# Optimization experiments

Hardware: AMD Instinct MI355X
Metric: run time of the kernel (lower is better)

Reference implementation:

```python
import jax, jax.numpy as jnp
import numpy as np
import math

EMBED_DIM = 1024
NUM_HEADS = 16
HEAD_DIM = EMBED_DIM // NUM_HEADS
BATCH = 2
SEQ = 2048


def setup_inputs() -> dict:
    key = jax.random.key(0)
    ks = jax.random.split(key, 9)
    s = 1.0 / math.sqrt(EMBED_DIM)
    return {
        "x": jax.random.normal(ks[0], (BATCH, SEQ, EMBED_DIM), jnp.float32),
        "Wq": jax.random.normal(ks[1], (EMBED_DIM, EMBED_DIM), jnp.float32) * s,
        "bq": jnp.zeros((EMBED_DIM,), jnp.float32),
        "Wk": jax.random.normal(ks[2], (EMBED_DIM, EMBED_DIM), jnp.float32) * s,
        "bk": jnp.zeros((EMBED_DIM,), jnp.float32),
        "Wv": jax.random.normal(ks[3], (EMBED_DIM, EMBED_DIM), jnp.float32) * s,
        "bv": jnp.zeros((EMBED_DIM,), jnp.float32),
        "Wo": jax.random.normal(ks[4], (EMBED_DIM, EMBED_DIM), jnp.float32) * s,
        "bo": jnp.zeros((EMBED_DIM,), jnp.float32),
    }


def _rope_tables(seq_len, dim, dtype):
    inv_freq = 1.0 / (10000.0 ** (jnp.arange(0, dim, 2, dtype=jnp.float32) / dim))
    t = jnp.arange(seq_len, dtype=jnp.float32)
    freqs = jnp.einsum("i,j->ij", t, inv_freq)          # [S, D/2]
    emb = jnp.concatenate([freqs, freqs], axis=-1)       # [S, D]
    return jnp.cos(emb).astype(dtype), jnp.sin(emb).astype(dtype)


def _rotate_half(x):
    x1, x2 = jnp.split(x, 2, axis=-1)
    return jnp.concatenate([-x2, x1], axis=-1)


def _apply_rope(x, cos, sin):
    # x: [B, S, H, D]; cos/sin: [S, D] -> broadcast over batch & heads
    cos = cos[None, :, None, :]
    sin = sin[None, :, None, :]
    return x * cos + _rotate_half(x) * sin


def reference(x, Wq, bq, Wk, bk, Wv, bv, Wo, bo):
    B, S, E = x.shape
    H, D = NUM_HEADS, HEAD_DIM
    q = (x @ Wq + bq).reshape(B, S, H, D)
    k = (x @ Wk + bk).reshape(B, S, H, D)
    v = (x @ Wv + bv).reshape(B, S, H, D)
    cos, sin = _rope_tables(S, D, x.dtype)
    q = _apply_rope(q, cos, sin)
    k = _apply_rope(k, cos, sin)
    scale = 1.0 / math.sqrt(D)
    # scores: [B, H, S, S]
    scores = jnp.einsum("bqhd,bkhd->bhqk", q, k) * scale
    attn = jax.nn.softmax(scores, axis=-1)
    ctx = jnp.einsum("bhqk,bkhd->bqhd", attn, v).reshape(B, S, E)
    return ctx @ Wo + bo
```

## Files before the change

kernel.cpp:

```cpp
#include <hip/hip_runtime.h>
#include <math.h>

#define B_ 2
#define S_ 2048
#define E_ 1024
#define H_ 16
#define D_ 64
#define M_ (B_*S_)

typedef _Float16 f16x8  __attribute__((ext_vector_type(8)));
typedef _Float16 f16x4v __attribute__((ext_vector_type(4)));
typedef __fp16   h16x2  __attribute__((ext_vector_type(2)));
typedef float    f32x4  __attribute__((ext_vector_type(4)));

__device__ __forceinline__ ushort f2h(float f) {
    _Float16 h = (_Float16)f;
    return __builtin_bit_cast(ushort, h);
}

__device__ __forceinline__ void gload_lds16(const ushort* g, ushort* l) {
    __builtin_amdgcn_global_load_lds(
        (const __attribute__((address_space(1))) unsigned int*)g,
        (__attribute__((address_space(3))) unsigned int*)l, 16, 0, 0);
}

__device__ __forceinline__ float exp2_fast(float x) {
    return __builtin_amdgcn_exp2f(x);
}

__global__ void prep_kernel(const float* __restrict__ x,
                            const float* __restrict__ W0, const float* __restrict__ W1,
                            const float* __restrict__ W2, const float* __restrict__ W3,
                            ushort* __restrict__ xf, ushort* __restrict__ WT,
                            float* __restrict__ ct, float* __restrict__ st)
{
    const int bid = blockIdx.x;
    const int tid = threadIdx.x;
    __shared__ float tile[32][33];

    if (bid < 4096) {
        const int z = bid >> 10, rem = bid & 1023;
        const int k0 = (rem >> 5) * 32, nb = (rem & 31) * 32;
        const float* W = (z == 0) ? W0 : (z == 1) ? W1 : (z == 2) ? W2 : W3;
        const size_t zoff = (size_t)z * E_ * E_;
        const int tx = tid & 31, ty = tid >> 5;
        #pragma unroll
        for (int i = 0; i < 4; i++) {
            int r = i * 8 + ty;
            tile[r][tx] = W[(size_t)(k0 + r) * E_ + nb + tx];
        }
        __syncthreads();
        #pragma unroll
        for (int i = 0; i < 4; i++) {
            int r = i * 8 + ty;
            WT[zoff + (size_t)(nb + r) * E_ + k0 + tx] = f2h(tile[tx][r]);
        }
    } else if (bid < 8192) {
        const int i = (bid - 4096) * 1024 + tid * 4;
        float4 v = *(const float4*)&x[i];
        *(ushort4*)&xf[i] = make_ushort4(f2h(v.x), f2h(v.y), f2h(v.z), f2h(v.w));
    } else {
        const int i = (bid - 8192) * 256 + tid;
        const int j = i & 31, pos = i >> 5;
        float invf = (float)pow(10000.0, -(double)j / 32.0);
        float ang  = (float)pos * invf;
        ct[i] = (float)cos((double)ang);
        st[i] = (float)sin((double)ang);
    }
}

#define GBM 128
#define GBN 128
#define GBK 32
#define LOG2E 1.44269504088896340736f

__global__ __launch_bounds__(256, 3)
void gemm_f16(const ushort* __restrict__ A, const ushort* __restrict__ WTp,
              const float* __restrict__ b0, const float* __restrict__ b1,
              const float* __restrict__ b2,
              const float* __restrict__ ct, const float* __restrict__ st,
              ushort* __restrict__ outQ, ushort* __restrict__ outK,
              ushort* __restrict__ outV, float* __restrict__ outF,
              int force_mode)
{
    __shared__ __align__(16) ushort lA[3][GBM * GBK];
    __shared__ __align__(16) ushort lB[3][GBN * GBK];

    const int tid  = threadIdx.x;
    const int wv   = tid >> 6, lane = tid & 63;
    const int c    = lane & 15, qd = lane >> 4;
    const int rh   = wv >> 1, chn = wv & 1;

    const int mode = (force_mode >= 0) ? force_mode : (int)blockIdx.z;
    const size_t zoff = (force_mode >= 0) ? 0 : (size_t)blockIdx.z * (E_ * E_);
    const ushort* Bt = WTp + zoff;

    const int m0 = (blockIdx.x & 31) * GBM;
    const int n0 = (blockIdx.x >> 5) * GBN;

    const ushort* gsrc = (wv < 2) ? A : Bt;
    const int rowbase = ((wv < 2) ? m0 : n0) + (wv & 1) * 64;
    const int lofs = (wv & 1) * 64 * GBK;
    const int srow = lane >> 2;
    const int soct = (lane & 3) * 8;

    f32x4 acc[4][4] = {};

    #pragma unroll
    for (int pt = 0; pt < 2; pt++) {
        ushort* dst = ((wv < 2) ? &lA[pt][0] : &lB[pt][0]) + lofs;
        const int k0i = pt * GBK;
        #pragma unroll
        for (int cc = 0; cc < 4; cc++) {
            const ushort* g = gsrc + (size_t)(rowbase + cc * 16 + srow) * E_ + k0i + soct;
            gload_lds16(g, dst + cc * 512);
        }
    }
    __builtin_amdgcn_s_waitcnt(0x0F74);
    __builtin_amdgcn_s_barrier();

    for (int t = 0; t < E_ / GBK; t++) {
        if (t + 2 < E_ / GBK) {
            const int bi = (t + 2) % 3;
            const int k0i = (t + 2) * GBK;
            ushort* dst = ((wv < 2) ? &lA[bi][0] : &lB[bi][0]) + lofs;
            #pragma unroll
            for (int cc = 0; cc < 4; cc++) {
                const ushort* g = gsrc + (size_t)(rowbase + cc * 16 + srow) * E_ + k0i + soct;
                gload_lds16(g, dst + cc * 512);
            }
        }

        const ushort* Ab = lA[t % 3];
        const ushort* Bb = lB[t % 3];

        f16x8 af[4], bf[4];
        #pragma unroll
        for (int mt = 0; mt < 4; mt++)
            af[mt] = *(const f16x8*)&Ab[(rh * 64 + mt * 16 + c) * GBK + qd * 8];
        #pragma unroll
        for (int nt = 0; nt < 4; nt++)
            bf[nt] = *(const f16x8*)&Bb[(chn * 64 + nt * 16 + c) * GBK + qd * 8];
        #pragma unroll
        for (int mt = 0; mt < 4; mt++)
            #pragma unroll
            for (int nt = 0; nt < 4; nt++)
                acc[mt][nt] = __builtin_amdgcn_mfma_f32_16x16x32_f16(af[mt], bf[nt], acc[mt][nt], 0, 0, 0);

        if (t < E_ / GBK - 2) {
            __builtin_amdgcn_s_waitcnt(0x0F74);
            __builtin_amdgcn_s_barrier();
        } else if (t == E_ / GBK - 2) {
            __builtin_amdgcn_s_waitcnt(0x0F70);
            __builtin_amdgcn_s_barrier();
        }
    }

    const float* bias = (mode == 0) ? b0 : (mode == 1) ? b1 : (mode == 2) ? b2 : b0;
    const int colbase = n0 + chn * 64;

    if (mode == 3) {
        #pragma unroll
        for (int mt = 0; mt < 4; mt++)
            #pragma unroll
            for (int r = 0; r < 4; r++) {
                const int row = m0 + rh * 64 + mt * 16 + qd * 4 + r;
                #pragma unroll
                for (int nt = 0; nt < 4; nt++) {
                    const int col = colbase + nt * 16 + c;
                    outF[(size_t)row * E_ + col] = acc[mt][nt][r] + bias[col];
                }
            }
    } else if (mode == 2) {
        const int hd = colbase >> 6;
        const int xr = (c >> 2) & 3;
        #pragma unroll
        for (int mt = 0; mt < 4; mt++)
            #pragma unroll
            for (int r = 0; r < 4; r++) {
                const int row = m0 + rh * 64 + mt * 16 + qd * 4 + r;
                const int bb = row >> 11, sl = row & (S_ - 1);
                const int g  = sl >> 5, k32 = sl & 31;
                const int q2 = (k32 >> 2) & 3, kh = k32 >> 4, kj = k32 & 3;
                const size_t base = (size_t)(bb * H_ + hd) * (S_ * D_)
                                  + g * 2048 + ((q2 ^ xr) << 3) + kh * 4 + kj;
                #pragma unroll
                for (int nt = 0; nt < 4; nt++) {
                    const int d = nt * 16 + c;
                    outV[base + (size_t)d * 32] = f2h(acc[mt][nt][r] + bias[colbase + d]);
                }
            }
    } else {
        ushort* O = (mode == 0) ? outQ : outK;
        const float sc = (mode == 0) ? 0.125f * LOG2E : 1.0f;
        #pragma unroll
        for (int mt = 0; mt < 4; mt++)
            #pragma unroll
            for (int r = 0; r < 4; r++) {
                const int row = m0 + rh * 64 + mt * 16 + qd * 4 + r;
                const int pos = row & (S_ - 1);
                const int sw = row & 7;
                #pragma unroll
                for (int p = 0; p < 2; p++) {
                    const int j32 = p * 16 + c;
                    const float cth = ct[pos * 32 + j32], sth = st[pos * 32 + j32];
                    const float v1 = acc[mt][p][r]     + bias[colbase + p * 16 + c];
                    const float v2 = acc[mt][p + 2][r] + bias[colbase + (p + 2) * 16 + c];
                    const float o1 = (v1 * cth - v2 * sth) * sc;
                    const float o2 = (v2 * cth + v1 * sth) * sc;
                    const int cd1 = p * 16 + c, cd2 = cd1 + 32;
                    O[(size_t)row * E_ + colbase + (((cd1 >> 3) ^ sw) * 8) + (cd1 & 7)] = f2h(o1);
                    O[(size_t)row * E_ + colbase + (((cd2 >> 3) ^ sw) * 8) + (cd2 & 7)] = f2h(o2);
                }
            }
    }
}

__global__ __launch_bounds__(256, 3)
void attn_mfma(const ushort* __restrict__ Qf, const ushort* __restrict__ Kf,
               const ushort* __restrict__ Vfg, ushort* __restrict__ ctxf)
{
    __shared__ __align__(16) ushort L[24576];

    const int tid = threadIdx.x;
    const int wv = tid >> 6, lane = tid & 63;
    const int c = lane & 15, qd = lane >> 4;
    const int cs = c & 7;

    const int xcd = blockIdx.x & 7, ii = blockIdx.x >> 3;
    const int bh = xcd * 4 + (ii & 3);
    const int qtb = ii >> 2;
    const int b = bh >> 4, h = bh & 15;
    const int q0 = qtb * 64;

    const size_t qrow0 = (size_t)b * S_ + q0;
    const size_t krow0 = (size_t)b * S_;
    const size_t vbase = (size_t)bh * (S_ * D_);

    const int l8 = lane >> 3, l7 = lane & 7;

    #pragma unroll
    for (int j = 0; j < 2; j++) {
        const int row = wv * 16 + j * 8 + l8;
        gload_lds16(Qf + (qrow0 + row) * E_ + h * 64 + l7 * 8, &L[wv * 1024 + j * 512]);
    }
    __syncthreads();
    f16x8 qfrag[4][2];
    #pragma unroll
    for (int qt = 0; qt < 4; qt++)
        #pragma unroll
        for (int kc = 0; kc < 2; kc++)
            qfrag[qt][kc] = *(const f16x8*)&L[(qt * 16 + c) * 64 + (((kc * 4 + qd) ^ cs) * 8)];
    __syncthreads();

    f32x4 acc[4][4] = {};
    float lsum[4] = {0.f, 0.f, 0.f, 0.f};

    ushort* const myL = &L[wv * 6144];
    const int vxo = (qd ^ ((c >> 2) & 3)) << 3;

    const ushort* kst0 = Kf + (krow0 + wv * 32 + l8) * E_ + h * 64 + l7 * 8;
    const ushort* kst1 = kst0 + 8 * E_;
    const ushort* vstA = Vfg + vbase + (size_t)wv * 2048 + lane * 8;
    const ushort* vstB = vstA + 512;

    gload_lds16(kst0, myL);
    gload_lds16(kst1, myL + 512);
    gload_lds16(vstA, myL + 2048);
    gload_lds16(vstB, myL + 2560);
    kst0 += 16 * E_; kst1 += 16 * E_; vstA += 1024; vstB += 1024;

    #pragma unroll 1
    for (int T = 0; T < 16; T++) {
        uint4 bfu[4];

        {
            ushort* vd = myL + 2048 + (T & 1) * 2048 + 1024;
            gload_lds16(kst0, myL + 1024);
            gload_lds16(kst1, myL + 1536);
            gload_lds16(vstA, vd);
            gload_lds16(vstB, vd + 512);
            kst0 += 112 * E_; kst1 += 112 * E_; vstA += 7168; vstB += 7168;
            __builtin_amdgcn_s_waitcnt(0x0F74);

            const ushort* kb = myL;
            f16x8 kf0 = *(const f16x8*)&kb[c * 64 + ((qd ^ cs) * 8)];
            f16x8 kf1 = *(const f16x8*)&kb[c * 64 + (((4 + qd) ^ cs) * 8)];
            f32x4 sv[4];
            __builtin_amdgcn_s_setprio(1);
            #pragma unroll
            for (int qt = 0; qt < 4; qt++) {
                f32x4 s = {};
                s = __builtin_amdgcn_mfma_f32_16x16x32_f16(kf0, qfrag[qt][0], s, 0, 0, 0);
                sv[qt] = __builtin_amdgcn_mfma_f32_16x16x32_f16(kf1, qfrag[qt][1], s, 0, 0, 0);
            }
            __builtin_amdgcn_s_setprio(0);
            #pragma unroll
            for (int qt = 0; qt < 4; qt++) {
                const float p0 = exp2_fast(sv[qt][0]), p1 = exp2_fast(sv[qt][1]);
                const float p2 = exp2_fast(sv[qt][2]), p3 = exp2_fast(sv[qt][3]);
                lsum[qt] += (p0 + p1) + (p2 + p3);
                bfu[qt].x = __builtin_bit_cast(unsigned int, __builtin_amdgcn_cvt_pkrtz(p0, p1));
                bfu[qt].y = __builtin_bit_cast(unsigned int, __builtin_amdgcn_cvt_pkrtz(p2, p3));
            }
        }

        {
            if (T < 15) {
                ushort* vd = myL + 2048 + ((T + 1) & 1) * 2048;
                gload_lds16(kst0, myL);
                gload_lds16(kst1, myL + 512);
                gload_lds16(vstA, vd);
                gload_lds16(vstB, vd + 512);
                kst0 += 16 * E_; kst1 += 16 * E_; vstA += 1024; vstB += 1024;
                __builtin_amdgcn_s_waitcnt(0x0F74);
            } else {
                __builtin_amdgcn_s_waitcnt(0x0F70);
            }

            const ushort* kb = myL + 1024;
            f16x8 kf0 = *(const f16x8*)&kb[c * 64 + ((qd ^ cs) * 8)];
            f16x8 kf1 = *(const f16x8*)&kb[c * 64 + (((4 + qd) ^ cs) * 8)];
            f32x4 sv[4];
            __builtin_amdgcn_s_setprio(1);
            #pragma unroll
            for (int qt = 0; qt < 4; qt++) {
                f32x4 s = {};
                s = __builtin_amdgcn_mfma_f32_16x16x32_f16(kf0, qfrag[qt][0], s, 0, 0, 0);
                sv[qt] = __builtin_amdgcn_mfma_f32_16x16x32_f16(kf1, qfrag[qt][1], s, 0, 0, 0);
            }
            __builtin_amdgcn_s_setprio(0);
            #pragma unroll
            for (int qt = 0; qt < 4; qt++) {
                const float p0 = exp2_fast(sv[qt][0]), p1 = exp2_fast(sv[qt][1]);
                const float p2 = exp2_fast(sv[qt][2]), p3 = exp2_fast(sv[qt][3]);
                lsum[qt] += (p0 + p1) + (p2 + p3);
                bfu[qt].z = __builtin_bit_cast(unsigned int, __builtin_amdgcn_cvt_pkrtz(p0, p1));
                bfu[qt].w = __builtin_bit_cast(unsigned int, __builtin_amdgcn_cvt_pkrtz(p2, p3));
            }
        }

        const ushort* vb = myL + 2048 + (T & 1) * 2048;
        __builtin_amdgcn_s_setprio(1);
        #pragma unroll
        for (int dt = 0; dt < 4; dt++) {
            f16x8 vfr = *(const f16x8*)&vb[(dt * 16 + c) * 32 + vxo];
            #pragma unroll
            for (int qt = 0; qt < 4; qt++)
                acc[dt][qt] = __builtin_amdgcn_mfma_f32_16x16x32_f16(
                    vfr, __builtin_bit_cast(f16x8, bfu[qt]), acc[dt][qt], 0, 0, 0);
        }
        __builtin_amdgcn_s_setprio(0);
    }

    __syncthreads();

    float* red = (float*)&L[0];
    float* lsr = (float*)&L[8192];

    #pragma unroll
    for (int qt = 0; qt < 4; qt++) {
        float v = lsum[qt];
        v += __shfl_xor(v, 16);
        v += __shfl_xor(v, 32);
        lsum[qt] = v;
    }
    if (lane < 16) {
        #pragma unroll
        for (int qt = 0; qt < 4; qt++) lsr[wv * 64 + qt * 16 + lane] = lsum[qt];
    }

    f32x4 own[4];
    #pragma unroll
    for (int qt = 0; qt < 4; qt++)
        own[qt] = (wv == 0) ? acc[0][qt] : (wv == 1) ? acc[1][qt]
                : (wv == 2) ? acc[2][qt] : acc[3][qt];

    #pragma unroll
    for (int r = 1; r < 4; r++) {
        const int ds = (wv + r) & 3;
        #pragma unroll
        for (int qt = 0; qt < 4; qt++) {
            f32x4 sv = (ds == 0) ? acc[0][qt] : (ds == 1) ? acc[1][qt]
                     : (ds == 2) ? acc[2][qt] : acc[3][qt];
            *(f32x4*)&red[ds * 1024 + qt * 256 + lane * 4] = sv;
        }
        __syncthreads();
        #pragma unroll
        for (int qt = 0; qt < 4; qt++)
            own[qt] += *(const f32x4*)&red[wv * 1024 + qt * 256 + lane * 4];
        if (r < 3) __syncthreads();
    }

    float inv[4];
    #pragma unroll
    for (int qt = 0; qt < 4; qt++) {
        const int q = qt * 16 + c;
        inv[qt] = 1.0f / (lsr[q] + lsr[64 + q] + lsr[128 + q] + lsr[192 + q]);
    }

    const size_t obase = qrow0 * E_ + h * 64 + wv * 16 + qd * 4;
    #pragma unroll
    for (int qt = 0; qt < 4; qt++) {
        f32x4 v = own[qt];
        const float iq = inv[qt];
        ushort4 o = make_ushort4(f2h(v[0] * iq), f2h(v[1] * iq),
                                 f2h(v[2] * iq), f2h(v[3] * iq));
        *(ushort4*)&ctxf[obase + (size_t)(qt * 16 + c) * E_] = o;
    }
}

extern "C" void kernel_launch(void* const* d_in, const int* in_sizes, int n_in,
                              void* d_out, int out_size, void* d_ws, size_t ws_size,
                              hipStream_t stream)
{
    const float* x  = (const float*)d_in[0];
    const float* Wq = (const float*)d_in[1];
    const float* bq = (const float*)d_in[2];
    const float* Wk = (const float*)d_in[3];
    const float* bk = (const float*)d_in[4];
    const float* Wv = (const float*)d_in[5];
    const float* bv = (const float*)d_in[6];
    const float* Wo = (const float*)d_in[7];
    const float* bo = (const float*)d_in[8];
    float* out = (float*)d_out;

    ushort* Qb = (ushort*)d_ws;
    ushort* Kb = Qb + (size_t)M_ * E_;
    ushort* Vf = Kb + (size_t)M_ * E_;
    ushort* xf = Vf + (size_t)M_ * E_;
    ushort* WT = xf + (size_t)M_ * E_;
    float*  ct = (float*)(WT + (size_t)4 * E_ * E_);
    float*  st = ct + S_ * 32;
    ushort* ctxf = Qb;

    hipLaunchKernelGGL(prep_kernel, dim3(8448), dim3(256), 0, stream,
                       x, Wq, Wk, Wv, Wo, xf, WT, ct, st);

    hipLaunchKernelGGL(gemm_f16, dim3(256, 1, 3), dim3(256), 0, stream,
                       xf, WT, bq, bk, bv, ct, st,
                       Qb, Kb, Vf, (float*)nullptr, -1);

    hipLaunchKernelGGL(attn_mfma, dim3(B_ * H_ * (S_ / 64)), dim3(256), 0, stream,
                       Qb, Kb, Vf, ctxf);

    hipLaunchKernelGGL(gemm_f16, dim3(256), dim3(256), 0, stream,
                       ctxf, WT + (size_t)3 * E_ * E_, bo, bo, bo, ct, st,
                       (ushort*)nullptr, (ushort*)nullptr, (ushort*)nullptr, out, 3);
}
```

Measured before the change: 182.4 us.

## Add dedicated 64x128-tile output projection GEMM and coarsen prep kernel blocks

The output projection moves from the shared 128x128 gemm_f16 path (256 blocks) into a new gemm_proj kernel. It uses 64x128 tiles, so it launches 512 blocks and fills more of the GPU's compute units. In gemm_proj three of the four waves stage the A and B tiles into LDS, and each wave computes a 64x32 slice. The prep kernel also does more work per block: each weight-transpose block now handles two 32-row k tiles, and each x-conversion block converts four float4 chunks, which cuts the grid from 8448 to 3328 blocks. The trade-offs are lower per-block arithmetic intensity in the projection GEMM and an extra barrier per transpose tile.

```diff
diff --git a/kernel.cpp b/kernel.cpp
--- a/kernel.cpp
+++ b/kernel.cpp
@@ -38,29 +38,38 @@
     const int tid = threadIdx.x;
     __shared__ float tile[32][33];
 
-    if (bid < 4096) {
-        const int z = bid >> 10, rem = bid & 1023;
-        const int k0 = (rem >> 5) * 32, nb = (rem & 31) * 32;
+    if (bid < 2048) {
+        const int z = bid >> 9, rem = bid & 511;
+        const int kp = rem >> 5, nb = (rem & 31) * 32;
         const float* W = (z == 0) ? W0 : (z == 1) ? W1 : (z == 2) ? W2 : W3;
         const size_t zoff = (size_t)z * E_ * E_;
         const int tx = tid & 31, ty = tid >> 5;
         #pragma unroll
-        for (int i = 0; i < 4; i++) {
-            int r = i * 8 + ty;
-            tile[r][tx] = W[(size_t)(k0 + r) * E_ + nb + tx];
-        }
-        __syncthreads();
-        #pragma unroll
-        for (int i = 0; i < 4; i++) {
-            int r = i * 8 + ty;
-            WT[zoff + (size_t)(nb + r) * E_ + k0 + tx] = f2h(tile[tx][r]);
-        }
-    } else if (bid < 8192) {
-        const int i = (bid - 4096) * 1024 + tid * 4;
-        float4 v = *(const float4*)&x[i];
-        *(ushort4*)&xf[i] = make_ushort4(f2h(v.x), f2h(v.y), f2h(v.z), f2h(v.w));
+        for (int kk = 0; kk < 2; kk++) {
+            const int k0 = kp * 64 + kk * 32;
+            #pragma unroll
+            for (int i = 0; i < 4; i++) {
+                int r = i * 8 + ty;
+                tile[r][tx] = W[(size_t)(k0 + r) * E_ + nb + tx];
+            }
+            __syncthreads();
+            #pragma unroll
+            for (int i = 0; i < 4; i++) {
+                int r = i * 8 + ty;
+                WT[zoff + (size_t)(nb + r) * E_ + k0 + tx] = f2h(tile[tx][r]);
+            }
+            __syncthreads();
+        }
+    } else if (bid < 3072) {
+        const int base = (bid - 2048) * 4096 + tid * 4;
+        #pragma unroll
+        for (int j = 0; j < 4; j++) {
+            const int i = base + j * 1024;
+            float4 v = *(const float4*)&x[i];
+            *(ushort4*)&xf[i] = make_ushort4(f2h(v.x), f2h(v.y), f2h(v.z), f2h(v.w));
+        }
     } else {
-        const int i = (bid - 8192) * 256 + tid;
+        const int i = (bid - 3072) * 256 + tid;
         const int j = i & 31, pos = i >> 5;
         float invf = (float)pow(10000.0, -(double)j / 32.0);
         float ang  = (float)pos * invf;
@@ -80,8 +89,7 @@
               const float* __restrict__ b2,
               const float* __restrict__ ct, const float* __restrict__ st,
               ushort* __restrict__ outQ, ushort* __restrict__ outK,
-              ushort* __restrict__ outV, float* __restrict__ outF,
-              int force_mode)
+              ushort* __restrict__ outV)
 {
     __shared__ __align__(16) ushort lA[3][GBM * GBK];
     __shared__ __align__(16) ushort lB[3][GBN * GBK];
@@ -91,8 +99,8 @@
     const int c    = lane & 15, qd = lane >> 4;
     const int rh   = wv >> 1, chn = wv & 1;
 
-    const int mode = (force_mode >= 0) ? force_mode : (int)blockIdx.z;
-    const size_t zoff = (force_mode >= 0) ? 0 : (size_t)blockIdx.z * (E_ * E_);
+    const int mode = (int)blockIdx.z;
+    const size_t zoff = (size_t)blockIdx.z * (E_ * E_);
     const ushort* Bt = WTp + zoff;
 
     const int m0 = (blockIdx.x & 31) * GBM;
@@ -156,22 +164,10 @@
         }
     }
 
-    const float* bias = (mode == 0) ? b0 : (mode == 1) ? b1 : (mode == 2) ? b2 : b0;
+    const float* bias = (mode == 0) ? b0 : (mode == 1) ? b1 : b2;
     const int colbase = n0 + chn * 64;
 
-    if (mode == 3) {
-        #pragma unroll
-        for (int mt = 0; mt < 4; mt++)
-            #pragma unroll
-            for (int r = 0; r < 4; r++) {
-                const int row = m0 + rh * 64 + mt * 16 + qd * 4 + r;
-                #pragma unroll
-                for (int nt = 0; nt < 4; nt++) {
-                    const int col = colbase + nt * 16 + c;
-                    outF[(size_t)row * E_ + col] = acc[mt][nt][r] + bias[col];
-                }
-            }
-    } else if (mode == 2) {
+    if (mode == 2) {
         const int hd = colbase >> 6;
         const int xr = (c >> 2) & 3;
         #pragma unroll
@@ -217,6 +213,94 @@
 }
 
 __global__ __launch_bounds__(256, 3)
+void gemm_proj(const ushort* __restrict__ A, const ushort* __restrict__ WTp,
+               const float* __restrict__ bo, float* __restrict__ outF)
+{
+    __shared__ __align__(16) ushort lA[3][64 * GBK];
+    __shared__ __align__(16) ushort lB[3][GBN * GBK];
+
+    const int tid  = threadIdx.x;
+    const int wv   = tid >> 6, lane = tid & 63;
+    const int c    = lane & 15, qd = lane >> 4;
+
+    const int m0 = (blockIdx.x & 63) * 64;
+    const int n0 = (blockIdx.x >> 6) * GBN;
+
+    const bool stager = (wv < 3);
+    const ushort* gsrc = (wv == 0) ? A : WTp;
+    const int rowbase = (wv == 0) ? m0 : (n0 + (wv - 1) * 64);
+    const int lofs = (wv == 0) ? 0 : (wv - 1) * 64 * GBK;
+    const int srow = lane >> 2;
+    const int soct = (lane & 3) * 8;
+
+    f32x4 acc[4][2] = {};
+
+    #pragma unroll
+    for (int pt = 0; pt < 2; pt++) {
+        if (stager) {
+            ushort* dst = ((wv == 0) ? &lA[pt][0] : &lB[pt][0]) + lofs;
+            const int k0i = pt * GBK;
+            #pragma unroll
+            for (int cc = 0; cc < 4; cc++) {
+                const ushort* g = gsrc + (size_t)(rowbase + cc * 16 + srow) * E_ + k0i + soct;
+                gload_lds16(g, dst + cc * 512);
+            }
+        }
+    }
+    __builtin_amdgcn_s_waitcnt(0x0F74);
+    __builtin_amdgcn_s_barrier();
+
+    for (int t = 0; t < E_ / GBK; t++) {
+        if (t + 2 < E_ / GBK && stager) {
+            const int bi = (t + 2) % 3;
+            const int k0i = (t + 2) * GBK;
+            ushort* dst = ((wv == 0) ? &lA[bi][0] : &lB[bi][0]) + lofs;
+            #pragma unroll
+            for (int cc = 0; cc < 4; cc++) {
+                const ushort* g = gsrc + (size_t)(rowbase + cc * 16 + srow) * E_ + k0i + soct;
+                gload_lds16(g, dst + cc * 512);
+            }
+        }
+
+        const ushort* Ab = lA[t % 3];
+        const ushort* Bb = lB[t % 3];
+
+        f16x8 af[4], bf[2];
+        #pragma unroll
+        for (int mt = 0; mt < 4; mt++)
+            af[mt] = *(const f16x8*)&Ab[(mt * 16 + c) * GBK + qd * 8];
+        #pragma unroll
+        for (int nt = 0; nt < 2; nt++)
+            bf[nt] = *(const f16x8*)&Bb[(wv * 32 + nt * 16 + c) * GBK + qd * 8];
+        #pragma unroll
+        for (int mt = 0; mt < 4; mt++)
+            #pragma unroll
+            for (int nt = 0; nt < 2; nt++)
+                acc[mt][nt] = __builtin_amdgcn_mfma_f32_16x16x32_f16(af[mt], bf[nt], acc[mt][nt], 0, 0, 0);
+
+        if (t < E_ / GBK - 2) {
+            __builtin_amdgcn_s_waitcnt(0x0F74);
+            __builtin_amdgcn_s_barrier();
+        } else if (t == E_ / GBK - 2) {
+            __builtin_amdgcn_s_waitcnt(0x0F70);
+            __builtin_amdgcn_s_barrier();
+        }
+    }
+
+    #pragma unroll
+    for (int mt = 0; mt < 4; mt++)
+        #pragma unroll
+        for (int r = 0; r < 4; r++) {
+            const int row = m0 + mt * 16 + qd * 4 + r;
+            #pragma unroll
+            for (int nt = 0; nt < 2; nt++) {
+                const int col = n0 + wv * 32 + nt * 16 + c;
+                outF[(size_t)row * E_ + col] = acc[mt][nt][r] + bo[col];
+            }
+        }
+}
+
+__global__ __launch_bounds__(256, 3)
 void attn_mfma(const ushort* __restrict__ Qf, const ushort* __restrict__ Kf,
                const ushort* __restrict__ Vfg, ushort* __restrict__ ctxf)
 {
@@ -434,17 +518,16 @@
     float*  st = ct + S_ * 32;
     ushort* ctxf = Qb;
 
-    hipLaunchKernelGGL(prep_kernel, dim3(8448), dim3(256), 0, stream,
+    hipLaunchKernelGGL(prep_kernel, dim3(3328), dim3(256), 0, stream,
                        x, Wq, Wk, Wv, Wo, xf, WT, ct, st);
 
     hipLaunchKernelGGL(gemm_f16, dim3(256, 1, 3), dim3(256), 0, stream,
                        xf, WT, bq, bk, bv, ct, st,
-                       Qb, Kb, Vf, (float*)nullptr, -1);
+                       Qb, Kb, Vf);
 
     hipLaunchKernelGGL(attn_mfma, dim3(B_ * H_ * (S_ / 64)), dim3(256), 0, stream,
                        Qb, Kb, Vf, ctxf);
 
-    hipLaunchKernelGGL(gemm_f16, dim3(256), dim3(256), 0, stream,
-                       ctxf, WT + (size_t)3 * E_ * E_, bo, bo, bo, ct, st,
-                       (ushort*)nullptr, (ushort*)nullptr, (ushort*)nullptr, out, 3);
-}
+    hipLaunchKernelGGL(gemm_proj, dim3(512), dim3(256), 0, stream,
+                       ctxf, WT + (size_t)3 * E_ * E_, bo, out);
+}
```

Result: no change. 180.8 us (median of 2 runs) (-0.9%).
